# Optimization experiments

Hardware: AMD Instinct MI355X
Metric: run time of the kernel (lower is better)

Reference implementation:

```python
import jax, jax.numpy as jnp
import numpy as np

N = 50000   # graph_dim (nodes)
L = 4       # list_dim (config batch)
D = 128     # inp_dim == out_dim
KD = 16     # key_dim
E = 800000  # edges
DECAY = 0.7
N_ITER = 3
EPS = 1e-5


def setup_inputs() -> dict:
    key = jax.random.key(0)
    ks = jax.random.split(key, 12)
    w = lambda k, s: jax.random.normal(k, s, jnp.float32) * (1.0 / np.sqrt(s[0]))
    return {
        "x": jax.random.normal(ks[0], (L, N, D), jnp.float32),
        "edge_index": jax.random.randint(ks[1], (2, E), 0, N, jnp.int32),
        "edge_vals": jax.random.uniform(ks[2], (E,), jnp.float32),
        "sage_W": w(ks[3], (D, D)),
        "sage_b": jnp.zeros((D,), jnp.float32),
        "sage_aggW": w(ks[4], (D, D)),
        "sage_ln_g": jnp.ones((D,), jnp.float32),
        "sage_ln_b": jnp.zeros((D,), jnp.float32),
        "att_Wk": w(ks[5], (D, KD)),
        "att_Wq": w(ks[6], (D, KD)),
        "att_Wv": w(ks[7], (D, D)),
        "att_ln_g": jnp.ones((D,), jnp.float32),
        "att_ln_b": jnp.zeros((D,), jnp.float32),
        "lin1_W": w(ks[8], (2 * D, D)),
        "lin1_b": jnp.zeros((D,), jnp.float32),
        "lin2_W": w(ks[9], (D, D)),
        "lin2_b": jnp.zeros((D,), jnp.float32),
        "ln1_g": jnp.ones((D,), jnp.float32),
        "ln1_b": jnp.zeros((D,), jnp.float32),
        "ln2_g": jnp.ones((D,), jnp.float32),
        "ln2_b": jnp.zeros((D,), jnp.float32),
    }


def layernorm(x, g, b):
    m = jnp.mean(x, axis=-1, keepdims=True)
    v = jnp.mean(jnp.square(x - m), axis=-1, keepdims=True)
    return (x - m) * jax.lax.rsqrt(v + EPS) * g + b


def spmm(edge_index, edge_vals, X):
    # sparse [N,N] @ dense [N,F] via COO gather-scatter
    rows, cols = edge_index[0], edge_index[1]
    return jax.ops.segment_sum(edge_vals[:, None] * X[cols], rows, num_segments=X.shape[0])


def reference(x, edge_index, edge_vals, sage_W, sage_b, sage_aggW, sage_ln_g, sage_ln_b,
              att_Wk, att_Wq, att_Wv, att_ln_g, att_ln_b,
              lin1_W, lin1_b, lin2_W, lin2_b, ln1_g, ln1_b, ln2_g, ln2_b):
    # --- SAGEConv ---
    proj = x @ sage_W + sage_b                              # [L,N,D]
    xt = jnp.transpose(x, (1, 0, 2)).reshape(N, L * D)      # [N, L*D]
    agg = spmm(edge_index, edge_vals, xt).reshape(N, L, D)
    agg = jnp.transpose(agg, (1, 0, 2))                     # [L,N,D]
    sage_out = layernorm(jax.nn.silu(proj + agg @ sage_aggW), sage_ln_g, sage_ln_b)

    # --- RetentiveAttention ---
    k = x @ att_Wk                                          # [L,N,KD]
    q = x @ att_Wq
    v = x @ att_Wv                                          # [L,N,D]
    weights = jnp.mean(k * q, axis=-1, keepdims=True)       # [L,N,1]
    iter_w = weights[..., 0].T                              # [N,L]
    for _ in range(1, N_ITER):
        iter_w = spmm(edge_index, edge_vals, iter_w * DECAY)
        weights = weights + iter_w.T[..., None]
    att_out = layernorm(v * weights, att_ln_g, att_ln_b)

    # --- GPS fusion ---
    h = jnp.concatenate([sage_out, att_out], axis=-1) @ lin1_W + lin1_b
    h = layernorm(jax.nn.silu(h), ln1_g, ln1_b)
    h = h @ lin2_W + lin2_b
    out = layernorm(jax.nn.silu(h + x), ln2_g, ln2_b)
    return out
```

## Files before the change

### kernel.cpp

```cpp
#include <hip/hip_runtime.h>
#include <hip/hip_fp16.h>

#define NN 50000
#define LL 4
#define DD 128
#define KDIM 16
#define EE 800000
#define MM (NN * LL)
#define DECAYF 0.7f
#define EPSF 1e-5f
#define SCAN_CHUNK 512
#define SCAN_NBLK ((NN + SCAN_CHUNK - 1) / SCAN_CHUNK)

typedef __attribute__((ext_vector_type(8))) short s16x8;
typedef __attribute__((ext_vector_type(4))) float fx4;

__device__ __forceinline__ short f2bf(float x) {
    unsigned u = __float_as_uint(x);
    u += 0x7fffu + ((u >> 16) & 1u);
    return (short)(u >> 16);
}
__device__ __forceinline__ float bf2f(short h) {
    return __uint_as_float(((unsigned)(unsigned short)h) << 16);
}
__device__ __forceinline__ float silu(float y) {
    return y * __builtin_amdgcn_rcpf(1.f + __expf(-y));
}

__global__ void k_zero(int* p, int n) {
    int i = blockIdx.x * 256 + threadIdx.x;
    if (i < n) p[i] = 0;
}
__global__ void k_hist(const int* __restrict__ rows, int* __restrict__ counts) {
    int e = blockIdx.x * 256 + threadIdx.x;
    if (e < EE) atomicAdd(&counts[rows[e]], 1);
}
__global__ void k_scan1(const int* __restrict__ counts, int* __restrict__ offs, int* __restrict__ csum) {
    __shared__ int s[SCAN_CHUNK];
    int i = blockIdx.x * SCAN_CHUNK + threadIdx.x;
    int v = (i < NN) ? counts[i] : 0;
    s[threadIdx.x] = v;
    __syncthreads();
    for (int off = 1; off < SCAN_CHUNK; off <<= 1) {
        int t = (threadIdx.x >= off) ? s[threadIdx.x - off] : 0;
        __syncthreads();
        s[threadIdx.x] += t;
        __syncthreads();
    }
    if (i < NN) offs[i] = s[threadIdx.x] - v;
    if (threadIdx.x == SCAN_CHUNK - 1) csum[blockIdx.x] = s[SCAN_CHUNK - 1];
}
__global__ void k_scan2(int* __restrict__ csum) {
    __shared__ int s[128];
    int v = (threadIdx.x < SCAN_NBLK) ? csum[threadIdx.x] : 0;
    s[threadIdx.x] = v;
    __syncthreads();
    for (int off = 1; off < 128; off <<= 1) {
        int t = (threadIdx.x >= off) ? s[threadIdx.x - off] : 0;
        __syncthreads();
        s[threadIdx.x] += t;
        __syncthreads();
    }
    if (threadIdx.x < SCAN_NBLK) csum[threadIdx.x] = s[threadIdx.x] - v;
}
__global__ void k_scan3(int* __restrict__ offs, const int* __restrict__ csum, int* __restrict__ cursor) {
    int i = blockIdx.x * SCAN_CHUNK + threadIdx.x;
    if (i < NN) {
        int v = offs[i] + csum[blockIdx.x];
        offs[i] = v;
        cursor[i] = v;
    } else if (i == NN) {
        offs[NN] = EE;
    }
}
__global__ void k_fill(const int* __restrict__ rows, const int* __restrict__ cols,
                       const float* __restrict__ vals,
                       int* __restrict__ cursor, int2* __restrict__ cpack) {
    int e = blockIdx.x * 256 + threadIdx.x;
    if (e < EE) {
        int r = rows[e];
        int pos = atomicAdd(&cursor[r], 1);
        cpack[pos] = make_int2(cols[e], __float_as_int(vals[e]));
    }
}

__global__ __launch_bounds__(256) void k_xhalf(const float* __restrict__ x, __half* __restrict__ xh) {
    size_t i = (size_t)blockIdx.x * 256 + threadIdx.x;
    float4 v = *reinterpret_cast<const float4*>(x + i * 4);
    __half2 h0 = __floats2half2_rn(v.x, v.y);
    __half2 h1 = __floats2half2_rn(v.z, v.w);
    __half2* d = reinterpret_cast<__half2*>(xh + i * 4);
    d[0] = h0;
    d[1] = h1;
}

__global__ __launch_bounds__(128) void k_agg_h(const int* __restrict__ offs,
                                               const int2* __restrict__ cpack,
                                               const __half* __restrict__ xh,
                                               float* __restrict__ agg) {
    int n = blockIdx.x;
    int hf = threadIdx.x >> 6;
    int lane = threadIdx.x & 63;
    int s = offs[n], e = offs[n + 1];
    const __half* b0 = xh + (size_t)(2 * hf) * NN * DD + lane * 2;
    const __half* b1 = xh + (size_t)(2 * hf + 1) * NN * DD + lane * 2;
    float a00 = 0.f, a01 = 0.f, a10 = 0.f, a11 = 0.f;
    #pragma unroll 2
    for (int p = s; p < e; p++) {
        int2 cw = cpack[p];
        int c = cw.x;
        float wv = __int_as_float(cw.y);
        float2 f0 = __half22float2(*reinterpret_cast<const __half2*>(b0 + (size_t)c * DD));
        float2 f1 = __half22float2(*reinterpret_cast<const __half2*>(b1 + (size_t)c * DD));
        a00 += wv * f0.x; a01 += wv * f0.y;
        a10 += wv * f1.x; a11 += wv * f1.y;
    }
    *reinterpret_cast<float2*>(agg + ((size_t)(2 * hf) * NN + n) * DD + lane * 2)     = make_float2(a00, a01);
    *reinterpret_cast<float2*>(agg + ((size_t)(2 * hf + 1) * NN + n) * DD + lane * 2) = make_float2(a10, a11);
}

__global__ __launch_bounds__(128) void k_agg_f(const int* __restrict__ offs,
                                               const int2* __restrict__ cpack,
                                               const float* __restrict__ x,
                                               float* __restrict__ agg) {
    int n = blockIdx.x;
    int tid = threadIdx.x;
    int s = offs[n], e = offs[n + 1];
    float a0 = 0.f, a1 = 0.f, a2 = 0.f, a3 = 0.f;
    for (int p = s; p < e; p++) {
        int2 cw = cpack[p];
        int c = cw.x;
        float w = __int_as_float(cw.y);
        a0 += w * x[((size_t)(0 * NN + c)) * DD + tid];
        a1 += w * x[((size_t)(1 * NN + c)) * DD + tid];
        a2 += w * x[((size_t)(2 * NN + c)) * DD + tid];
        a3 += w * x[((size_t)(3 * NN + c)) * DD + tid];
    }
    agg[((size_t)(0 * NN + n)) * DD + tid] = a0;
    agg[((size_t)(1 * NN + n)) * DD + tid] = a1;
    agg[((size_t)(2 * NN + n)) * DD + tid] = a2;
    agg[((size_t)(3 * NN + n)) * DD + tid] = a3;
}

__global__ void k_wprep(const float* __restrict__ sW, const float* __restrict__ aW,
                        const float* __restrict__ vW, const float* __restrict__ w1,
                        const float* __restrict__ w2,
                        const float* __restrict__ wk, const float* __restrict__ wq,
                        short* __restrict__ out) {
    int b = blockIdx.x;
    if (b < 384) {
        const float* src; short* h; short* l; int K; int base;
        if (b < 64)       { src = sW; h = out;          l = out + 16384;  K = 128; base = b; }
        else if (b < 128) { src = aW; h = out + 32768;  l = out + 49152;  K = 128; base = b - 64; }
        else if (b < 192) { src = vW; h = out + 65536;  l = out + 81920;  K = 128; base = b - 128; }
        else if (b < 320) { src = w1; h = out + 98304;  l = out + 131072; K = 256; base = b - 192; }
        else              { src = w2; h = out + 163840; l = out + 180224; K = 128; base = b - 320; }
        int idx = base * 256 + threadIdx.x;
        int k = idx >> 7, n = idx & 127;
        float v = src[idx];
        short hh = f2bf(v);
        h[n * K + k] = hh;
        l[n * K + k] = f2bf(v - bf2f(hh));
    } else {
        int idx = (b - 384) * 256 + threadIdx.x;
        int j = idx >> 7, k = idx & 127;
        float v = (j < 16) ? wk[k * KDIM + j] : wq[k * KDIM + (j - 16)];
        short hh = f2bf(v);
        out[196608 + j * 128 + k] = hh;
        out[200704 + j * 128 + k] = f2bf(v - bf2f(hh));
    }
}

__device__ __forceinline__ void stage64(const float* __restrict__ src, int rowbase,
                                        short* __restrict__ h, short* __restrict__ l, int tid) {
    int row = tid >> 2, ko = (tid & 3) * 32;
    const float* gp = src + (size_t)(rowbase + row) * DD + ko;
    short* dh = h + row * 136 + ko;
    short* dl = l + row * 136 + ko;
    #pragma unroll
    for (int j = 0; j < 4; j++) {
        float4 a = *reinterpret_cast<const float4*>(gp + j * 8);
        float4 b = *reinterpret_cast<const float4*>(gp + j * 8 + 4);
        float v[8] = {a.x, a.y, a.z, a.w, b.x, b.y, b.z, b.w};
        s16x8 hv, lv;
        #pragma unroll
        for (int e = 0; e < 8; e++) {
            short hh = f2bf(v[e]);
            hv[e] = hh;
            lv[e] = f2bf(v[e] - bf2f(hh));
        }
        *(s16x8*)(dh + j * 8) = hv;
        *(s16x8*)(dl + j * 8) = lv;
    }
}
__device__ __forceinline__ void stage64h(const float* __restrict__ src, int rowbase,
                                         short* __restrict__ h, int tid) {
    int row = tid >> 2, ko = (tid & 3) * 32;
    const float* gp = src + (size_t)(rowbase + row) * DD + ko;
    short* dh = h + row * 136 + ko;
    #pragma unroll
    for (int j = 0; j < 4; j++) {
        float4 a = *reinterpret_cast<const float4*>(gp + j * 8);
        float4 b = *reinterpret_cast<const float4*>(gp + j * 8 + 4);
        s16x8 hv;
        hv[0] = f2bf(a.x); hv[1] = f2bf(a.y); hv[2] = f2bf(a.z); hv[3] = f2bf(a.w);
        hv[4] = f2bf(b.x); hv[5] = f2bf(b.y); hv[6] = f2bf(b.z); hv[7] = f2bf(b.w);
        *(s16x8*)(dh + j * 8) = hv;
    }
}

__device__ __forceinline__ void mfma_pass1(const short* __restrict__ a0,
                                           const short* __restrict__ Wh,
                                           int wlen, int koff, int w, int l16, int kg,
                                           fx4 acc[4][2]) {
    #pragma unroll
    for (int ks = 0; ks < 4; ks++) {
        s16x8 ah[4];
        #pragma unroll
        for (int mt = 0; mt < 4; mt++)
            ah[mt] = *(const s16x8*)(a0 + (mt * 16 + l16) * 136 + ks * 32 + kg * 8);
        #pragma unroll
        for (int nt = 0; nt < 2; nt++) {
            int col = w * 32 + nt * 16 + l16;
            s16x8 bh = *(const s16x8*)(Wh + col * wlen + koff + ks * 32 + kg * 8);
            #pragma unroll
            for (int mt = 0; mt < 4; mt++)
                acc[mt][nt] = __builtin_amdgcn_mfma_f32_16x16x32_bf16(ah[mt], bh, acc[mt][nt], 0, 0, 0);
        }
    }
}

__global__ __launch_bounds__(256, 4) void k_sage2(
    const float* __restrict__ x,
    const short* __restrict__ aWh,
    const short* __restrict__ sWh,
    const short* __restrict__ kqh, const short* __restrict__ kql,
    const float* __restrict__ bias, const float* __restrict__ g, const float* __restrict__ bb,
    float* __restrict__ wt_total, float* __restrict__ iw0,
    float* __restrict__ io) {
    __shared__ __align__(16) short stg[2][64 * 136];
    float* fscr = (float*)&stg[0][0];
    short* sh = &stg[0][0];
    short* sl = &stg[1][0];
    const int rowbase = blockIdx.x * 64;
    const int tid = threadIdx.x;
    const int w = tid >> 6, lane = tid & 63;
    const int l16 = lane & 15, kg = lane >> 4;

    fx4 acc[4][2];
    #pragma unroll
    for (int mt = 0; mt < 4; mt++)
        #pragma unroll
        for (int nt = 0; nt < 2; nt++) acc[mt][nt] = (fx4){0.f, 0.f, 0.f, 0.f};

    stage64h(io, rowbase, sh, tid);
    __syncthreads();
    mfma_pass1(sh, aWh, 128, 0, w, l16, kg, acc);
    __syncthreads();

    stage64(x, rowbase, sh, sl, tid);
    __syncthreads();
    mfma_pass1(sh, sWh, 128, 0, w, l16, kg, acc);

    fx4 acck[2];
    acck[0] = (fx4){0.f, 0.f, 0.f, 0.f};
    acck[1] = (fx4){0.f, 0.f, 0.f, 0.f};
    #pragma unroll
    for (int ks = 0; ks < 4; ks++) {
        int ao = (w * 16 + l16) * 136 + ks * 32 + kg * 8;
        s16x8 ah = *(const s16x8*)(sh + ao);
        s16x8 al = *(const s16x8*)(sl + ao);
        #pragma unroll
        for (int nt = 0; nt < 2; nt++) {
            int bo = (nt * 16 + l16) * 128 + ks * 32 + kg * 8;
            s16x8 bh = *(const s16x8*)(kqh + bo);
            s16x8 bl = *(const s16x8*)(kql + bo);
            acck[nt] = __builtin_amdgcn_mfma_f32_16x16x32_bf16(ah, bh, acck[nt], 0, 0, 0);
            acck[nt] = __builtin_amdgcn_mfma_f32_16x16x32_bf16(ah, bl, acck[nt], 0, 0, 0);
            acck[nt] = __builtin_amdgcn_mfma_f32_16x16x32_bf16(al, bh, acck[nt], 0, 0, 0);
        }
    }
    #pragma unroll
    for (int r = 0; r < 4; r++) {
        float pr = acck[0][r] * acck[1][r];
        pr += __shfl_xor(pr, 1, 64);
        pr += __shfl_xor(pr, 2, 64);
        pr += __shfl_xor(pr, 4, 64);
        pr += __shfl_xor(pr, 8, 64);
        if (l16 == 0) {
            int row = w * 16 + kg * 4 + r;
            int m = rowbase + row;
            int l = m / NN, n = m - l * NN;
            float sv = pr * (1.f / 16.f);
            wt_total[n * LL + l] = sv;
            iw0[n * LL + l] = sv;
        }
    }
    __syncthreads();

    float bias_r[2];
    #pragma unroll
    for (int nt = 0; nt < 2; nt++) bias_r[nt] = bias[w * 32 + nt * 16 + l16];
    #pragma unroll
    for (int mt = 0; mt < 4; mt++) {
        #pragma unroll
        for (int r = 0; r < 4; r++) {
            int row = mt * 16 + kg * 4 + r;
            #pragma unroll
            for (int nt = 0; nt < 2; nt++) {
                int col = w * 32 + nt * 16 + l16;
                fscr[row * 129 + col] = silu(acc[mt][nt][r] + bias_r[nt]);
            }
        }
    }
    __syncthreads();
    {
        float g0 = g[lane], g1 = g[64 + lane];
        float b0 = bb[lane], b1 = bb[64 + lane];
        #pragma unroll 1
        for (int rr = 0; rr < 16; rr++) {
            int row = w * 16 + rr;
            size_t m = (size_t)rowbase + row;
            float y0 = fscr[row * 129 + lane], y1 = fscr[row * 129 + 64 + lane];
            float s = y0 + y1, q = y0 * y0 + y1 * y1;
            #pragma unroll
            for (int off = 32; off; off >>= 1) {
                s += __shfl_xor(s, off, 64);
                q += __shfl_xor(q, off, 64);
            }
            float mean = s * (1.f / 128.f);
            float var = fmaxf(q * (1.f / 128.f) - mean * mean, 0.f);
            float rstd = rsqrtf(var + EPSF);
            io[m * DD + lane]      = (y0 - mean) * rstd * g0 + b0;
            io[m * DD + 64 + lane] = (y1 - mean) * rstd * g1 + b1;
        }
    }
}

__global__ __launch_bounds__(256, 4) void k_lin12(
    const float* __restrict__ x,
    const short* __restrict__ Wvh,
    const float* __restrict__ wtbuf,
    const float* __restrict__ att_g, const float* __restrict__ att_b,
    const short* __restrict__ W1h,
    const float* __restrict__ b1v,
    const float* __restrict__ ln1g, const float* __restrict__ ln1b,
    const short* __restrict__ W2h,
    const float* __restrict__ b2v,
    const float* __restrict__ ln2g, const float* __restrict__ ln2b,
    float* __restrict__ io) {
    __shared__ __align__(16) short xt[64 * 136];
    __shared__ __align__(16) short atl[64 * 136];
    const int rowbase = blockIdx.x * 64;
    const int tid = threadIdx.x;
    const int w = tid >> 6, lane = tid & 63;
    const int l16 = lane & 15, kg = lane >> 4;

    float4 pf[8];
    {
        int row = tid >> 2, ko = (tid & 3) * 32;
        const float* gp = io + (size_t)(rowbase + row) * DD + ko;
        #pragma unroll
        for (int j = 0; j < 8; j++) pf[j] = *reinterpret_cast<const float4*>(gp + j * 4);
    }

    fx4 acc[4][2];
    #pragma unroll
    for (int mt = 0; mt < 4; mt++)
        #pragma unroll
        for (int nt = 0; nt < 2; nt++) acc[mt][nt] = (fx4){0.f, 0.f, 0.f, 0.f};

    stage64h(x, rowbase, xt, tid);
    __syncthreads();
    mfma_pass1(xt, Wvh, 128, 0, w, l16, kg, acc);
    #pragma unroll
    for (int mt = 0; mt < 4; mt++) {
        #pragma unroll
        for (int r = 0; r < 4; r++) {
            int row = mt * 16 + kg * 4 + r;
            int m = rowbase + row;
            int l = m / NN, n = m - l * NN;
            float ws = wtbuf[n * LL + l];
            #pragma unroll
            for (int nt = 0; nt < 2; nt++) {
                int col = w * 32 + nt * 16 + l16;
                atl[row * 136 + col] = f2bf(acc[mt][nt][r] * ws);
            }
        }
    }
    __syncthreads();

    {
        float g0 = att_g[lane], g1 = att_g[64 + lane];
        float b0 = att_b[lane], b1 = att_b[64 + lane];
        #pragma unroll 1
        for (int rr = 0; rr < 16; rr++) {
            int row = w * 16 + rr;
            float y0 = bf2f(atl[row * 136 + lane]), y1 = bf2f(atl[row * 136 + 64 + lane]);
            float s = y0 + y1, q = y0 * y0 + y1 * y1;
            #pragma unroll
            for (int off = 32; off; off >>= 1) {
                s += __shfl_xor(s, off, 64);
                q += __shfl_xor(q, off, 64);
            }
            float mean = s * (1.f / 128.f);
            float var = fmaxf(q * (1.f / 128.f) - mean * mean, 0.f);
            float rstd = rsqrtf(var + EPSF);
            atl[row * 136 + lane]      = f2bf((y0 - mean) * rstd * g0 + b0);
            atl[row * 136 + 64 + lane] = f2bf((y1 - mean) * rstd * g1 + b1);
        }
    }
    {
        int row = tid >> 2, ko = (tid & 3) * 32;
        short* dh = xt + row * 136 + ko;
        #pragma unroll
        for (int j = 0; j < 4; j++) {
            float4 a = pf[2 * j], b = pf[2 * j + 1];
            s16x8 hv;
            hv[0] = f2bf(a.x); hv[1] = f2bf(a.y); hv[2] = f2bf(a.z); hv[3] = f2bf(a.w);
            hv[4] = f2bf(b.x); hv[5] = f2bf(b.y); hv[6] = f2bf(b.z); hv[7] = f2bf(b.w);
            *(s16x8*)(dh + j * 8) = hv;
        }
    }
    __syncthreads();

    #pragma unroll
    for (int mt = 0; mt < 4; mt++)
        #pragma unroll
        for (int nt = 0; nt < 2; nt++) acc[mt][nt] = (fx4){0.f, 0.f, 0.f, 0.f};
    mfma_pass1(xt, W1h, 256, 0, w, l16, kg, acc);
    mfma_pass1(atl, W1h, 256, 128, w, l16, kg, acc);
    __syncthreads();

    {
        float bias_r[2];
        #pragma unroll
        for (int nt = 0; nt < 2; nt++) bias_r[nt] = b1v[w * 32 + nt * 16 + l16];
        #pragma unroll
        for (int mt = 0; mt < 4; mt++) {
            #pragma unroll
            for (int r = 0; r < 4; r++) {
                int row = mt * 16 + kg * 4 + r;
                #pragma unroll
                for (int nt = 0; nt < 2; nt++) {
                    int col = w * 32 + nt * 16 + l16;
                    atl[row * 136 + col] = f2bf(silu(acc[mt][nt][r] + bias_r[nt]));
                }
            }
        }
    }
    __syncthreads();
    {
        float g0 = ln1g[lane], g1 = ln1g[64 + lane];
        float b0 = ln1b[lane], b1 = ln1b[64 + lane];
        #pragma unroll 1
        for (int rr = 0; rr < 16; rr++) {
            int row = w * 16 + rr;
            float y0 = bf2f(atl[row * 136 + lane]), y1 = bf2f(atl[row * 136 + 64 + lane]);
            float s = y0 + y1, q = y0 * y0 + y1 * y1;
            #pragma unroll
            for (int off = 32; off; off >>= 1) {
                s += __shfl_xor(s, off, 64);
                q += __shfl_xor(q, off, 64);
            }
            float mean = s * (1.f / 128.f);
            float var = fmaxf(q * (1.f / 128.f) - mean * mean, 0.f);
            float rstd = rsqrtf(var + EPSF);
            atl[row * 136 + lane]      = f2bf((y0 - mean) * rstd * g0 + b0);
            atl[row * 136 + 64 + lane] = f2bf((y1 - mean) * rstd * g1 + b1);
        }
    }
    __syncthreads();

    #pragma unroll
    for (int mt = 0; mt < 4; mt++)
        #pragma unroll
        for (int nt = 0; nt < 2; nt++) acc[mt][nt] = (fx4){0.f, 0.f, 0.f, 0.f};
    mfma_pass1(atl, W2h, 128, 0, w, l16, kg, acc);
    {
        float bias_r[2];
        #pragma unroll
        for (int nt = 0; nt < 2; nt++) bias_r[nt] = b2v[w * 32 + nt * 16 + l16];
        #pragma unroll
        for (int mt = 0; mt < 4; mt++) {
            #pragma unroll
            for (int r = 0; r < 4; r++) {
                int row = mt * 16 + kg * 4 + r;
                size_t m = (size_t)rowbase + row;
                #pragma unroll
                for (int nt = 0; nt < 2; nt++) {
                    int col = w * 32 + nt * 16 + l16;
                    xt[row * 136 + col] = f2bf(silu(acc[mt][nt][r] + bias_r[nt] + x[m * DD + col]));
                }
            }
        }
    }
    __syncthreads();
    {
        float g0 = ln2g[lane], g1 = ln2g[64 + lane];
        float b0 = ln2b[lane], b1 = ln2b[64 + lane];
        #pragma unroll 1
        for (int rr = 0; rr < 16; rr++) {
            int row = w * 16 + rr;
            size_t m = (size_t)rowbase + row;
            float y0 = bf2f(xt[row * 136 + lane]), y1 = bf2f(xt[row * 136 + 64 + lane]);
            float s = y0 + y1, q = y0 * y0 + y1 * y1;
            #pragma unroll
            for (int off = 32; off; off >>= 1) {
                s += __shfl_xor(s, off, 64);
                q += __shfl_xor(q, off, 64);
            }
            float mean = s * (1.f / 128.f);
            float var = fmaxf(q * (1.f / 128.f) - mean * mean, 0.f);
            float rstd = rsqrtf(var + EPSF);
            io[m * DD + lane]      = (y0 - mean) * rstd * g0 + b0;
            io[m * DD + 64 + lane] = (y1 - mean) * rstd * g1 + b1;
        }
    }
}

__global__ __launch_bounds__(256) void k_spmm_w(const int* __restrict__ offs,
                                                const int2* __restrict__ cpack,
                                                const float* __restrict__ win, float* __restrict__ wout,
                                                float* __restrict__ wtot) {
    int i = blockIdx.x * 256 + threadIdx.x;
    if (i >= NN * LL) return;
    int n = i >> 2, l = i & 3;
    int s = offs[n], e = offs[n + 1];
    float a = 0.f;
    for (int p = s; p < e; p++) {
        int2 cw = cpack[p];
        a += __int_as_float(cw.y) * win[(cw.x << 2) | l];
    }
    a *= DECAYF;
    wout[i] = a;
    wtot[i] += a;
}

extern "C" void kernel_launch(void* const* d_in, const int* in_sizes, int n_in,
                              void* d_out, int out_size, void* d_ws, size_t ws_size,
                              hipStream_t stream) {
    const float* x        = (const float*)d_in[0];
    const int*   ei       = (const int*)d_in[1];
    const float* evals    = (const float*)d_in[2];
    const float* sage_W   = (const float*)d_in[3];
    const float* sage_b   = (const float*)d_in[4];
    const float* sage_aggW= (const float*)d_in[5];
    const float* sage_ln_g= (const float*)d_in[6];
    const float* sage_ln_b= (const float*)d_in[7];
    const float* att_Wk   = (const float*)d_in[8];
    const float* att_Wq   = (const float*)d_in[9];
    const float* att_Wv   = (const float*)d_in[10];
    const float* att_ln_g = (const float*)d_in[11];
    const float* att_ln_b = (const float*)d_in[12];
    const float* lin1_W   = (const float*)d_in[13];
    const float* lin1_b   = (const float*)d_in[14];
    const float* lin2_W   = (const float*)d_in[15];
    const float* lin2_b   = (const float*)d_in[16];
    const float* ln1_g    = (const float*)d_in[17];
    const float* ln1_b    = (const float*)d_in[18];
    const float* ln2_g    = (const float*)d_in[19];
    const float* ln2_b    = (const float*)d_in[20];

    const int* rows = ei;
    const int* cols = ei + EE;

    float* wt_total = (float*)d_ws;
    float* iw0      = wt_total + MM;
    float* iw1      = iw0 + MM;
    int*   counts   = (int*)(iw1 + MM);
    int*   offs     = counts + NN;
    int*   cursor   = offs + NN + 1;
    int*   csum     = cursor + NN;
    uintptr_t pc    = (uintptr_t)(csum + 128);
    pc = (pc + 15) & ~(uintptr_t)15;
    int2*  cpack    = (int2*)pc;
    uintptr_t pw    = (uintptr_t)(cpack + EE);
    pw = (pw + 15) & ~(uintptr_t)15;
    short* wbf      = (short*)pw;
    uintptr_t ph    = (uintptr_t)(wbf + 204800);
    ph = (ph + 255) & ~(uintptr_t)255;
    __half* xh      = (__half*)ph;
    size_t need_h   = (ph - (uintptr_t)d_ws) + (size_t)MM * DD * sizeof(__half);
    bool use_half   = ws_size >= need_h;
    float* io       = (float*)d_out;

    k_wprep<<<400, 256, 0, stream>>>(sage_W, sage_aggW, att_Wv, lin1_W, lin2_W,
                                     att_Wk, att_Wq, wbf);

    k_zero<<<(NN + 255) / 256, 256, 0, stream>>>(counts, NN);
    k_hist<<<(EE + 255) / 256, 256, 0, stream>>>(rows, counts);
    k_scan1<<<SCAN_NBLK, SCAN_CHUNK, 0, stream>>>(counts, offs, csum);
    k_scan2<<<1, 128, 0, stream>>>(csum);
    k_scan3<<<SCAN_NBLK, SCAN_CHUNK, 0, stream>>>(offs, csum, cursor);
    k_fill<<<(EE + 255) / 256, 256, 0, stream>>>(rows, cols, evals, cursor, cpack);

    if (use_half) {
        k_xhalf<<<(MM * DD / 4 + 255) / 256, 256, 0, stream>>>(x, xh);
        k_agg_h<<<NN, 128, 0, stream>>>(offs, cpack, xh, io);
    } else {
        k_agg_f<<<NN, 128, 0, stream>>>(offs, cpack, x, io);
    }

    k_sage2<<<MM / 64, 256, 0, stream>>>(
        x,
        wbf + 32768,
        wbf,
        wbf + 196608, wbf + 200704,
        sage_b, sage_ln_g, sage_ln_b,
        wt_total, iw0, io);

    k_spmm_w<<<(MM + 255) / 256, 256, 0, stream>>>(offs, cpack, iw0, iw1, wt_total);
    k_spmm_w<<<(MM + 255) / 256, 256, 0, stream>>>(offs, cpack, iw1, iw0, wt_total);

    k_lin12<<<MM / 64, 256, 0, stream>>>(
        x, wbf + 65536, wt_total, att_ln_g, att_ln_b,
        wbf + 98304, lin1_b, ln1_g, ln1_b,
        wbf + 163840, lin2_b, ln2_g, ln2_b,
        io);

    (void)in_sizes; (void)n_in; (void)out_size;
}
```

Before: 700.9 us.

## Give each wave its own 16-row tile and drop block barriers in dense kernels

Restructures the two dense MFMA kernels so that each wave owns 16 rows and all 128 output columns, using a private LDS slice instead of splitting columns across waves. Block-wide __syncthreads are replaced by a wave-local lgkmcnt wait. Layernorms are now computed straight from accumulator registers with 16-lane shuffles, which removes the LDS scratch round trips. In exchange, each wave now loads the full weight matrix from global memory, A-fragment reuse across row tiles is lost, and register pressure rises.

```diff
diff --git a/kernel.cpp b/kernel.cpp
--- a/kernel.cpp
+++ b/kernel.cpp
@@ -14,6 +14,12 @@
 
 typedef __attribute__((ext_vector_type(8))) short s16x8;
 typedef __attribute__((ext_vector_type(4))) float fx4;
+
+#define LDSFENCE() do { \
+    __builtin_amdgcn_sched_barrier(0); \
+    asm volatile("s_waitcnt lgkmcnt(0)" ::: "memory"); \
+    __builtin_amdgcn_sched_barrier(0); \
+} while (0)
 
 __device__ __forceinline__ short f2bf(float x) {
     unsigned u = __float_as_uint(x);
@@ -171,32 +177,10 @@
     }
 }
 
-__device__ __forceinline__ void stage64(const float* __restrict__ src, int rowbase,
-                                        short* __restrict__ h, short* __restrict__ l, int tid) {
-    int row = tid >> 2, ko = (tid & 3) * 32;
-    const float* gp = src + (size_t)(rowbase + row) * DD + ko;
-    short* dh = h + row * 136 + ko;
-    short* dl = l + row * 136 + ko;
-    #pragma unroll
-    for (int j = 0; j < 4; j++) {
-        float4 a = *reinterpret_cast<const float4*>(gp + j * 8);
-        float4 b = *reinterpret_cast<const float4*>(gp + j * 8 + 4);
-        float v[8] = {a.x, a.y, a.z, a.w, b.x, b.y, b.z, b.w};
-        s16x8 hv, lv;
-        #pragma unroll
-        for (int e = 0; e < 8; e++) {
-            short hh = f2bf(v[e]);
-            hv[e] = hh;
-            lv[e] = f2bf(v[e] - bf2f(hh));
-        }
-        *(s16x8*)(dh + j * 8) = hv;
-        *(s16x8*)(dl + j * 8) = lv;
-    }
-}
-__device__ __forceinline__ void stage64h(const float* __restrict__ src, int rowbase,
-                                         short* __restrict__ h, int tid) {
-    int row = tid >> 2, ko = (tid & 3) * 32;
-    const float* gp = src + (size_t)(rowbase + row) * DD + ko;
+__device__ __forceinline__ void wstage16h(const float* __restrict__ src, int rbase,
+                                          short* __restrict__ h, int lane) {
+    int row = lane >> 2, ko = (lane & 3) * 32;
+    const float* gp = src + (size_t)(rbase + row) * DD + ko;
     short* dh = h + row * 136 + ko;
     #pragma unroll
     for (int j = 0; j < 4; j++) {
@@ -208,24 +192,40 @@
         *(s16x8*)(dh + j * 8) = hv;
     }
 }
-
-__device__ __forceinline__ void mfma_pass1(const short* __restrict__ a0,
-                                           const short* __restrict__ Wh,
-                                           int wlen, int koff, int w, int l16, int kg,
-                                           fx4 acc[4][2]) {
+__device__ __forceinline__ void wstage16(const float* __restrict__ src, int rbase,
+                                         short* __restrict__ h, short* __restrict__ l, int lane) {
+    int row = lane >> 2, ko = (lane & 3) * 32;
+    const float* gp = src + (size_t)(rbase + row) * DD + ko;
+    short* dh = h + row * 136 + ko;
+    short* dl = l + row * 136 + ko;
+    #pragma unroll
+    for (int j = 0; j < 4; j++) {
+        float4 a = *reinterpret_cast<const float4*>(gp + j * 8);
+        float4 b = *reinterpret_cast<const float4*>(gp + j * 8 + 4);
+        float v[8] = {a.x, a.y, a.z, a.w, b.x, b.y, b.z, b.w};
+        s16x8 hv, lv;
+        #pragma unroll
+        for (int e = 0; e < 8; e++) {
+            short hh = f2bf(v[e]);
+            hv[e] = hh;
+            lv[e] = f2bf(v[e] - bf2f(hh));
+        }
+        *(s16x8*)(dh + j * 8) = hv;
+        *(s16x8*)(dl + j * 8) = lv;
+    }
+}
+
+__device__ __forceinline__ void mfma16(const short* __restrict__ a16,
+                                       const short* __restrict__ Wh,
+                                       int wlen, int koff, int l16, int kg,
+                                       fx4 acc[8]) {
     #pragma unroll
     for (int ks = 0; ks < 4; ks++) {
-        s16x8 ah[4];
-        #pragma unroll
-        for (int mt = 0; mt < 4; mt++)
-            ah[mt] = *(const s16x8*)(a0 + (mt * 16 + l16) * 136 + ks * 32 + kg * 8);
-        #pragma unroll
-        for (int nt = 0; nt < 2; nt++) {
-            int col = w * 32 + nt * 16 + l16;
-            s16x8 bh = *(const s16x8*)(Wh + col * wlen + koff + ks * 32 + kg * 8);
-            #pragma unroll
-            for (int mt = 0; mt < 4; mt++)
-                acc[mt][nt] = __builtin_amdgcn_mfma_f32_16x16x32_bf16(ah[mt], bh, acc[mt][nt], 0, 0, 0);
+        s16x8 ah = *(const s16x8*)(a16 + l16 * 136 + ks * 32 + kg * 8);
+        #pragma unroll
+        for (int nt = 0; nt < 8; nt++) {
+            s16x8 bh = *(const s16x8*)(Wh + (nt * 16 + l16) * wlen + koff + ks * 32 + kg * 8);
+            acc[nt] = __builtin_amdgcn_mfma_f32_16x16x32_bf16(ah, bh, acc[nt], 0, 0, 0);
         }
     }
 }
@@ -239,101 +239,89 @@
     float* __restrict__ wt_total, float* __restrict__ iw0,
     float* __restrict__ io) {
     __shared__ __align__(16) short stg[2][64 * 136];
-    float* fscr = (float*)&stg[0][0];
-    short* sh = &stg[0][0];
-    short* sl = &stg[1][0];
-    const int rowbase = blockIdx.x * 64;
     const int tid = threadIdx.x;
     const int w = tid >> 6, lane = tid & 63;
     const int l16 = lane & 15, kg = lane >> 4;
-
-    fx4 acc[4][2];
-    #pragma unroll
-    for (int mt = 0; mt < 4; mt++)
-        #pragma unroll
-        for (int nt = 0; nt < 2; nt++) acc[mt][nt] = (fx4){0.f, 0.f, 0.f, 0.f};
-
-    stage64h(io, rowbase, sh, tid);
-    __syncthreads();
-    mfma_pass1(sh, aWh, 128, 0, w, l16, kg, acc);
-    __syncthreads();
-
-    stage64(x, rowbase, sh, sl, tid);
-    __syncthreads();
-    mfma_pass1(sh, sWh, 128, 0, w, l16, kg, acc);
-
-    fx4 acck[2];
-    acck[0] = (fx4){0.f, 0.f, 0.f, 0.f};
-    acck[1] = (fx4){0.f, 0.f, 0.f, 0.f};
+    const int rbase = blockIdx.x * 64 + w * 16;
+    short* ph = &stg[0][w * (16 * 136)];
+    short* pl = &stg[1][w * (16 * 136)];
+
+    fx4 acc[8];
+    #pragma unroll
+    for (int nt = 0; nt < 8; nt++) acc[nt] = (fx4){0.f, 0.f, 0.f, 0.f};
+
+    wstage16h(io, rbase, ph, lane);
+    LDSFENCE();
+    mfma16(ph, aWh, 128, 0, l16, kg, acc);
+    LDSFENCE();
+
+    wstage16(x, rbase, ph, pl, lane);
+    LDSFENCE();
+    mfma16(ph, sWh, 128, 0, l16, kg, acc);
+
+    fx4 acck0 = (fx4){0.f, 0.f, 0.f, 0.f};
+    fx4 acck1 = (fx4){0.f, 0.f, 0.f, 0.f};
     #pragma unroll
     for (int ks = 0; ks < 4; ks++) {
-        int ao = (w * 16 + l16) * 136 + ks * 32 + kg * 8;
-        s16x8 ah = *(const s16x8*)(sh + ao);
-        s16x8 al = *(const s16x8*)(sl + ao);
-        #pragma unroll
-        for (int nt = 0; nt < 2; nt++) {
-            int bo = (nt * 16 + l16) * 128 + ks * 32 + kg * 8;
-            s16x8 bh = *(const s16x8*)(kqh + bo);
-            s16x8 bl = *(const s16x8*)(kql + bo);
-            acck[nt] = __builtin_amdgcn_mfma_f32_16x16x32_bf16(ah, bh, acck[nt], 0, 0, 0);
-            acck[nt] = __builtin_amdgcn_mfma_f32_16x16x32_bf16(ah, bl, acck[nt], 0, 0, 0);
-            acck[nt] = __builtin_amdgcn_mfma_f32_16x16x32_bf16(al, bh, acck[nt], 0, 0, 0);
-        }
+        int ao = l16 * 136 + ks * 32 + kg * 8;
+        s16x8 ah = *(const s16x8*)(ph + ao);
+        s16x8 al = *(const s16x8*)(pl + ao);
+        int bo0 = l16 * 128 + ks * 32 + kg * 8;
+        s16x8 bh0 = *(const s16x8*)(kqh + bo0);
+        s16x8 bl0 = *(const s16x8*)(kql + bo0);
+        acck0 = __builtin_amdgcn_mfma_f32_16x16x32_bf16(ah, bh0, acck0, 0, 0, 0);
+        acck0 = __builtin_amdgcn_mfma_f32_16x16x32_bf16(ah, bl0, acck0, 0, 0, 0);
+        acck0 = __builtin_amdgcn_mfma_f32_16x16x32_bf16(al, bh0, acck0, 0, 0, 0);
+        int bo1 = (16 + l16) * 128 + ks * 32 + kg * 8;
+        s16x8 bh1 = *(const s16x8*)(kqh + bo1);
+        s16x8 bl1 = *(const s16x8*)(kql + bo1);
+        acck1 = __builtin_amdgcn_mfma_f32_16x16x32_bf16(ah, bh1, acck1, 0, 0, 0);
+        acck1 = __builtin_amdgcn_mfma_f32_16x16x32_bf16(ah, bl1, acck1, 0, 0, 0);
+        acck1 = __builtin_amdgcn_mfma_f32_16x16x32_bf16(al, bh1, acck1, 0, 0, 0);
     }
     #pragma unroll
     for (int r = 0; r < 4; r++) {
-        float pr = acck[0][r] * acck[1][r];
+        float pr = acck0[r] * acck1[r];
         pr += __shfl_xor(pr, 1, 64);
         pr += __shfl_xor(pr, 2, 64);
         pr += __shfl_xor(pr, 4, 64);
         pr += __shfl_xor(pr, 8, 64);
         if (l16 == 0) {
-            int row = w * 16 + kg * 4 + r;
-            int m = rowbase + row;
+            int m = rbase + kg * 4 + r;
             int l = m / NN, n = m - l * NN;
             float sv = pr * (1.f / 16.f);
             wt_total[n * LL + l] = sv;
             iw0[n * LL + l] = sv;
         }
     }
-    __syncthreads();
-
-    float bias_r[2];
-    #pragma unroll
-    for (int nt = 0; nt < 2; nt++) bias_r[nt] = bias[w * 32 + nt * 16 + l16];
-    #pragma unroll
-    for (int mt = 0; mt < 4; mt++) {
-        #pragma unroll
-        for (int r = 0; r < 4; r++) {
-            int row = mt * 16 + kg * 4 + r;
-            #pragma unroll
-            for (int nt = 0; nt < 2; nt++) {
-                int col = w * 32 + nt * 16 + l16;
-                fscr[row * 129 + col] = silu(acc[mt][nt][r] + bias_r[nt]);
-            }
-        }
-    }
-    __syncthreads();
-    {
-        float g0 = g[lane], g1 = g[64 + lane];
-        float b0 = bb[lane], b1 = bb[64 + lane];
-        #pragma unroll 1
-        for (int rr = 0; rr < 16; rr++) {
-            int row = w * 16 + rr;
-            size_t m = (size_t)rowbase + row;
-            float y0 = fscr[row * 129 + lane], y1 = fscr[row * 129 + 64 + lane];
-            float s = y0 + y1, q = y0 * y0 + y1 * y1;
-            #pragma unroll
-            for (int off = 32; off; off >>= 1) {
-                s += __shfl_xor(s, off, 64);
-                q += __shfl_xor(q, off, 64);
-            }
-            float mean = s * (1.f / 128.f);
-            float var = fmaxf(q * (1.f / 128.f) - mean * mean, 0.f);
-            float rstd = rsqrtf(var + EPSF);
-            io[m * DD + lane]      = (y0 - mean) * rstd * g0 + b0;
-            io[m * DD + 64 + lane] = (y1 - mean) * rstd * g1 + b1;
-        }
+
+    float br[8], gr[8], b2r[8];
+    #pragma unroll
+    for (int nt = 0; nt < 8; nt++) {
+        int col = nt * 16 + l16;
+        br[nt] = bias[col]; gr[nt] = g[col]; b2r[nt] = bb[col];
+    }
+    #pragma unroll
+    for (int nt = 0; nt < 8; nt++)
+        #pragma unroll
+        for (int r = 0; r < 4; r++)
+            acc[nt][r] = silu(acc[nt][r] + br[nt]);
+    #pragma unroll
+    for (int r = 0; r < 4; r++) {
+        float s = 0.f, q = 0.f;
+        #pragma unroll
+        for (int nt = 0; nt < 8; nt++) { float v = acc[nt][r]; s += v; q += v * v; }
+        s += __shfl_xor(s, 1, 64); q += __shfl_xor(q, 1, 64);
+        s += __shfl_xor(s, 2, 64); q += __shfl_xor(q, 2, 64);
+        s += __shfl_xor(s, 4, 64); q += __shfl_xor(q, 4, 64);
+        s += __shfl_xor(s, 8, 64); q += __shfl_xor(q, 8, 64);
+        float mu = s * (1.f / 128.f);
+        float var = fmaxf(q * (1.f / 128.f) - mu * mu, 0.f);
+        float rstd = rsqrtf(var + EPSF);
+        size_t m = (size_t)rbase + kg * 4 + r;
+        #pragma unroll
+        for (int nt = 0; nt < 8; nt++)
+            io[m * DD + nt * 16 + l16] = (acc[nt][r] - mu) * rstd * gr[nt] + b2r[nt];
     }
 }
 
@@ -351,68 +339,68 @@
     float* __restrict__ io) {
     __shared__ __align__(16) short xt[64 * 136];
     __shared__ __align__(16) short atl[64 * 136];
-    const int rowbase = blockIdx.x * 64;
     const int tid = threadIdx.x;
     const int w = tid >> 6, lane = tid & 63;
     const int l16 = lane & 15, kg = lane >> 4;
+    const int rbase = blockIdx.x * 64 + w * 16;
+    short* xw = xt + w * (16 * 136);
+    short* aw = atl + w * (16 * 136);
 
     float4 pf[8];
     {
-        int row = tid >> 2, ko = (tid & 3) * 32;
-        const float* gp = io + (size_t)(rowbase + row) * DD + ko;
+        int row = lane >> 2, ko = (lane & 3) * 32;
+        const float* gp = io + (size_t)(rbase + row) * DD + ko;
         #pragma unroll
         for (int j = 0; j < 8; j++) pf[j] = *reinterpret_cast<const float4*>(gp + j * 4);
     }
 
-    fx4 acc[4][2];
-    #pragma unroll
-    for (int mt = 0; mt < 4; mt++)
-        #pragma unroll
-        for (int nt = 0; nt < 2; nt++) acc[mt][nt] = (fx4){0.f, 0.f, 0.f, 0.f};
-
-    stage64h(x, rowbase, xt, tid);
-    __syncthreads();
-    mfma_pass1(xt, Wvh, 128, 0, w, l16, kg, acc);
-    #pragma unroll
-    for (int mt = 0; mt < 4; mt++) {
+    wstage16h(x, rbase, xw, lane);
+    LDSFENCE();
+    fx4 acc[8];
+    #pragma unroll
+    for (int nt = 0; nt < 8; nt++) acc[nt] = (fx4){0.f, 0.f, 0.f, 0.f};
+    mfma16(xw, Wvh, 128, 0, l16, kg, acc);
+
+    {
+        float ws[4];
         #pragma unroll
         for (int r = 0; r < 4; r++) {
-            int row = mt * 16 + kg * 4 + r;
-            int m = rowbase + row;
+            int m = rbase + kg * 4 + r;
             int l = m / NN, n = m - l * NN;
-            float ws = wtbuf[n * LL + l];
-            #pragma unroll
-            for (int nt = 0; nt < 2; nt++) {
-                int col = w * 32 + nt * 16 + l16;
-                atl[row * 136 + col] = f2bf(acc[mt][nt][r] * ws);
-            }
-        }
-    }
-    __syncthreads();
+            ws[r] = wtbuf[n * LL + l];
+        }
+        #pragma unroll
+        for (int nt = 0; nt < 8; nt++)
+            #pragma unroll
+            for (int r = 0; r < 4; r++) acc[nt][r] *= ws[r];
+        float gA[8], bA[8];
+        #pragma unroll
+        for (int nt = 0; nt < 8; nt++) {
+            int col = nt * 16 + l16;
+            gA[nt] = att_g[col]; bA[nt] = att_b[col];
+        }
+        #pragma unroll
+        for (int r = 0; r < 4; r++) {
+            float s = 0.f, q = 0.f;
+            #pragma unroll
+            for (int nt = 0; nt < 8; nt++) { float v = acc[nt][r]; s += v; q += v * v; }
+            s += __shfl_xor(s, 1, 64); q += __shfl_xor(q, 1, 64);
+            s += __shfl_xor(s, 2, 64); q += __shfl_xor(q, 2, 64);
+            s += __shfl_xor(s, 4, 64); q += __shfl_xor(q, 4, 64);
+            s += __shfl_xor(s, 8, 64); q += __shfl_xor(q, 8, 64);
+            float mu = s * (1.f / 128.f);
+            float var = fmaxf(q * (1.f / 128.f) - mu * mu, 0.f);
+            float rstd = rsqrtf(var + EPSF);
+            int row = kg * 4 + r;
+            #pragma unroll
+            for (int nt = 0; nt < 8; nt++)
+                aw[row * 136 + nt * 16 + l16] = f2bf((acc[nt][r] - mu) * rstd * gA[nt] + bA[nt]);
+        }
+    }
 
     {
-        float g0 = att_g[lane], g1 = att_g[64 + lane];
-        float b0 = att_b[lane], b1 = att_b[64 + lane];
-        #pragma unroll 1
-        for (int rr = 0; rr < 16; rr++) {
-            int row = w * 16 + rr;
-            float y0 = bf2f(atl[row * 136 + lane]), y1 = bf2f(atl[row * 136 + 64 + lane]);
-            float s = y0 + y1, q = y0 * y0 + y1 * y1;
-            #pragma unroll
-            for (int off = 32; off; off >>= 1) {
-                s += __shfl_xor(s, off, 64);
-                q += __shfl_xor(q, off, 64);
-            }
-            float mean = s * (1.f / 128.f);
-            float var = fmaxf(q * (1.f / 128.f) - mean * mean, 0.f);
-            float rstd = rsqrtf(var + EPSF);
-            atl[row * 136 + lane]      = f2bf((y0 - mean) * rstd * g0 + b0);
-            atl[row * 136 + 64 + lane] = f2bf((y1 - mean) * rstd * g1 + b1);
-        }
-    }
-    {
-        int row = tid >> 2, ko = (tid & 3) * 32;
-        short* dh = xt + row * 136 + ko;
+        int row = lane >> 2, ko = (lane & 3) * 32;
+        short* dh = xw + row * 136 + ko;
         #pragma unroll
         for (int j = 0; j < 4; j++) {
             float4 a = pf[2 * j], b = pf[2 * j + 1];
@@ -422,99 +410,77 @@
             *(s16x8*)(dh + j * 8) = hv;
         }
     }
-    __syncthreads();
-
-    #pragma unroll
-    for (int mt = 0; mt < 4; mt++)
-        #pragma unroll
-        for (int nt = 0; nt < 2; nt++) acc[mt][nt] = (fx4){0.f, 0.f, 0.f, 0.f};
-    mfma_pass1(xt, W1h, 256, 0, w, l16, kg, acc);
-    mfma_pass1(atl, W1h, 256, 128, w, l16, kg, acc);
-    __syncthreads();
+    LDSFENCE();
+
+    #pragma unroll
+    for (int nt = 0; nt < 8; nt++) acc[nt] = (fx4){0.f, 0.f, 0.f, 0.f};
+    mfma16(xw, W1h, 256, 0, l16, kg, acc);
+    mfma16(aw, W1h, 256, 128, l16, kg, acc);
 
     {
-        float bias_r[2];
-        #pragma unroll
-        for (int nt = 0; nt < 2; nt++) bias_r[nt] = b1v[w * 32 + nt * 16 + l16];
-        #pragma unroll
-        for (int mt = 0; mt < 4; mt++) {
+        float b1r[8], g1r[8], bb1[8];
+        #pragma unroll
+        for (int nt = 0; nt < 8; nt++) {
+            int col = nt * 16 + l16;
+            b1r[nt] = b1v[col]; g1r[nt] = ln1g[col]; bb1[nt] = ln1b[col];
+        }
+        #pragma unroll
+        for (int nt = 0; nt < 8; nt++)
+            #pragma unroll
+            for (int r = 0; r < 4; r++) acc[nt][r] = silu(acc[nt][r] + b1r[nt]);
+        #pragma unroll
+        for (int r = 0; r < 4; r++) {
+            float s = 0.f, q = 0.f;
+            #pragma unroll
+            for (int nt = 0; nt < 8; nt++) { float v = acc[nt][r]; s += v; q += v * v; }
+            s += __shfl_xor(s, 1, 64); q += __shfl_xor(q, 1, 64);
+            s += __shfl_xor(s, 2, 64); q += __shfl_xor(q, 2, 64);
+            s += __shfl_xor(s, 4, 64); q += __shfl_xor(q, 4, 64);
+            s += __shfl_xor(s, 8, 64); q += __shfl_xor(q, 8, 64);
+            float mu = s * (1.f / 128.f);
+            float var = fmaxf(q * (1.f / 128.f) - mu * mu, 0.f);
+            float rstd = rsqrtf(var + EPSF);
+            int row = kg * 4 + r;
+            #pragma unroll
+            for (int nt = 0; nt < 8; nt++)
+                aw[row * 136 + nt * 16 + l16] = f2bf((acc[nt][r] - mu) * rstd * g1r[nt] + bb1[nt]);
+        }
+    }
+    LDSFENCE();
+
+    #pragma unroll
+    for (int nt = 0; nt < 8; nt++) acc[nt] = (fx4){0.f, 0.f, 0.f, 0.f};
+    mfma16(aw, W2h, 128, 0, l16, kg, acc);
+    {
+        float b2r[8], g2r[8], bb2[8];
+        #pragma unroll
+        for (int nt = 0; nt < 8; nt++) {
+            int col = nt * 16 + l16;
+            b2r[nt] = b2v[col]; g2r[nt] = ln2g[col]; bb2[nt] = ln2b[col];
+        }
+        #pragma unroll
+        for (int nt = 0; nt < 8; nt++)
             #pragma unroll
             for (int r = 0; r < 4; r++) {
-                int row = mt * 16 + kg * 4 + r;
-                #pragma unroll
-                for (int nt = 0; nt < 2; nt++) {
-                    int col = w * 32 + nt * 16 + l16;
-                    atl[row * 136 + col] = f2bf(silu(acc[mt][nt][r] + bias_r[nt]));
-                }
+                size_t m = (size_t)rbase + kg * 4 + r;
+                acc[nt][r] = silu(acc[nt][r] + b2r[nt] + x[m * DD + nt * 16 + l16]);
             }
-        }
-    }
-    __syncthreads();
-    {
-        float g0 = ln1g[lane], g1 = ln1g[64 + lane];
-        float b0 = ln1b[lane], b1 = ln1b[64 + lane];
-        #pragma unroll 1
-        for (int rr = 0; rr < 16; rr++) {
-            int row = w * 16 + rr;
-            float y0 = bf2f(atl[row * 136 + lane]), y1 = bf2f(atl[row * 136 + 64 + lane]);
-            float s = y0 + y1, q = y0 * y0 + y1 * y1;
-            #pragma unroll
-            for (int off = 32; off; off >>= 1) {
-                s += __shfl_xor(s, off, 64);
-                q += __shfl_xor(q, off, 64);
-            }
-            float mean = s * (1.f / 128.f);
-            float var = fmaxf(q * (1.f / 128.f) - mean * mean, 0.f);
+        #pragma unroll
+        for (int r = 0; r < 4; r++) {
+            float s = 0.f, q = 0.f;
+            #pragma unroll
+            for (int nt = 0; nt < 8; nt++) { float v = acc[nt][r]; s += v; q += v * v; }
+            s += __shfl_xor(s, 1, 64); q += __shfl_xor(q, 1, 64);
+            s += __shfl_xor(s, 2, 64); q += __shfl_xor(q, 2, 64);
+            s += __shfl_xor(s, 4, 64); q += __shfl_xor(q, 4, 64);
+            s += __shfl_xor(s, 8, 64); q += __shfl_xor(q, 8, 64);
+            float mu = s * (1.f / 128.f);
+            float var = fmaxf(q * (1.f / 128.f) - mu * mu, 0.f);
             float rstd = rsqrtf(var + EPSF);
-            atl[row * 136 + lane]      = f2bf((y0 - mean) * rstd * g0 + b0);
-            atl[row * 136 + 64 + lane] = f2bf((y1 - mean) * rstd * g1 + b1);
-        }
-    }
-    __syncthreads();
-
-    #pragma unroll
-    for (int mt = 0; mt < 4; mt++)
-        #pragma unroll
-        for (int nt = 0; nt < 2; nt++) acc[mt][nt] = (fx4){0.f, 0.f, 0.f, 0.f};
-    mfma_pass1(atl, W2h, 128, 0, w, l16, kg, acc);
-    {
-        float bias_r[2];
-        #pragma unroll
-        for (int nt = 0; nt < 2; nt++) bias_r[nt] = b2v[w * 32 + nt * 16 + l16];
-        #pragma unroll
-        for (int mt = 0; mt < 4; mt++) {
-            #pragma unroll
-            for (int r = 0; r < 4; r++) {
-                int row = mt * 16 + kg * 4 + r;
-                size_t m = (size_t)rowbase + row;
-                #pragma unroll
-                for (int nt = 0; nt < 2; nt++) {
-                    int col = w * 32 + nt * 16 + l16;
-                    xt[row * 136 + col] = f2bf(silu(acc[mt][nt][r] + bias_r[nt] + x[m * DD + col]));
-                }
-            }
-        }
-    }
-    __syncthreads();
-    {
-        float g0 = ln2g[lane], g1 = ln2g[64 + lane];
-        float b0 = ln2b[lane], b1 = ln2b[64 + lane];
-        #pragma unroll 1
-        for (int rr = 0; rr < 16; rr++) {
-            int row = w * 16 + rr;
-            size_t m = (size_t)rowbase + row;
-            float y0 = bf2f(xt[row * 136 + lane]), y1 = bf2f(xt[row * 136 + 64 + lane]);
-            float s = y0 + y1, q = y0 * y0 + y1 * y1;
-            #pragma unroll
-            for (int off = 32; off; off >>= 1) {
-                s += __shfl_xor(s, off, 64);
-                q += __shfl_xor(q, off, 64);
-            }
-            float mean = s * (1.f / 128.f);
-            float var = fmaxf(q * (1.f / 128.f) - mean * mean, 0.f);
-            float rstd = rsqrtf(var + EPSF);
-            io[m * DD + lane]      = (y0 - mean) * rstd * g0 + b0;
-            io[m * DD + 64 + lane] = (y1 - mean) * rstd * g1 + b1;
+            size_t m = (size_t)rbase + kg * 4 + r;
+            #pragma unroll
+            for (int nt = 0; nt < 8; nt++)
+                io[m * DD + nt * 16 + l16] = (acc[nt][r] - mu) * rstd * g2r[nt] + bb2[nt];
         }
     }
 }
```

Result: slower. 848.2 us (+21.0%).
